# Kernel optimization log

Measured on AMD Instinct MI355X. Metric: run time of the kernel, lower is better.

The kernel has to match this reference:

```python
import jax, jax.numpy as jnp
import numpy as np

NH = 32          # nh * 2 neighbors per point (init nh=16)
P_REDUCTION = 0.5


def setup_inputs() -> dict:
    key = jax.random.key(0)
    k1, k2 = jax.random.split(key)
    x = jax.random.normal(k1, (2, 8192, 256), dtype=jnp.float32)       # [b, n, e]
    coords = jax.random.normal(k2, (2, 2, 8192, 1), dtype=jnp.float32) # [b, c, n, 1]
    return {"x": x, "coords": coords}


def _knn_gather(x, coords):
    """Return features of the NH nearest neighbors of each point: [b, n, NH, e]."""
    cs = coords[..., 0]                                   # [b, c, n]
    sq = jnp.sum(cs * cs, axis=1)                         # [b, n]
    # squared euclidean distances [b, n, n]
    d2 = sq[:, :, None] + sq[:, None, :] - 2.0 * jnp.einsum('bcn,bcm->bnm', cs, cs)
    d2 = jax.lax.stop_gradient(d2)                        # indices are non-differentiable
    _, nn_idx = jax.lax.top_k(-d2, NH)                    # [b, n, NH] nearest points
    # gather neighbor features: [b, 1, n, e] indexed with [b, n, NH, 1] -> [b, n, NH, e]
    x_nh = jnp.take_along_axis(x[:, None, :, :], nn_idx[..., None], axis=2)
    return x_nh


def _forward(x, coords):
    b, n, e = x.shape
    x_nh = _knn_gather(x, coords)                         # [b, n, NH, e]
    # unbiased std over the neighbor dim (torch.std default, ddof=1)
    mean_nh = jnp.mean(x_nh, axis=-2, keepdims=True)
    local_s = jnp.sqrt(jnp.sum((x_nh - mean_nh) ** 2, axis=-2) / (NH - 1))  # [b, n, e]
    global_m = jnp.abs(jnp.mean(x, axis=1))               # [b, e]
    local_dist = jnp.sum(local_s / global_m[:, None, :], axis=-1)           # [b, n]
    n_keep = int((1.0 - P_REDUCTION) * n)
    _, keep_idx = jax.lax.top_k(local_dist, n_keep)       # [b, n_keep], sorted desc
    x_out = jnp.take_along_axis(x, keep_idx[:, :, None], axis=1)            # [b, n_keep, e]
    coords_out = jnp.take_along_axis(coords, keep_idx[:, None, :, None], axis=2)  # [b, c, n_keep, 1]
    return x_out, coords_out, local_dist


def reference(x, coords):
    return _forward(x, coords)
```

## Files before the change

### kernel.cpp

```cpp
#include <hip/hip_runtime.h>

#define NN 8192
#define EE 256
#define KNH 32
#define NKEEP 4096
#define NCX 64
#define NCELL 4096
#define CNT_MIN 48

typedef unsigned long long u64;
typedef unsigned int u32;


__device__ __forceinline__ int cellof(float v) {
    const int q = (int)floorf((v + 4.6f) * (64.0f / 9.2f));
    return min(max(q, 0), NCX - 1);
}

__global__ void __launch_bounds__(1024) k_pre(const float* __restrict__ coords,
                                              const float* __restrict__ x,
                                              int* __restrict__ start,
                                              float2* __restrict__ sc,
                                              int* __restrict__ sj,
                                              float* __restrict__ part) {
    __shared__ int cnt[NCELL];
    __shared__ int wsum[16];
    const int blk = blockIdx.x;
    if (blk >= 2) {
        const int unit  = (blk - 2) * 4 + (threadIdx.x >> 8);
        const int b     = unit >> 5;
        const int chunk = unit & 31;
        const int t     = threadIdx.x & 255;
        const float* xp = x + ((size_t)b * NN + (size_t)chunk * 256) * EE + t;
        float s = 0.0f;
        for (int i = 0; i < 256; ++i) s += xp[(size_t)i * EE];
        part[((size_t)b * 32 + chunk) * EE + t] = s;
        return;
    }
    const int b = blk, t = threadIdx.x;
    const int lane = t & 63, wv = t >> 6;
#pragma unroll
    for (int k = 0; k < 4; ++k) cnt[k * 1024 + t] = 0;
    __syncthreads();
#pragma unroll
    for (int k = 0; k < 8; ++k) {
        const int i = k * 1024 + t;
        const float xv = coords[(size_t)b * 2 * NN + i];
        const float yv = coords[(size_t)b * 2 * NN + NN + i];
        atomicAdd(&cnt[cellof(xv) * NCX + cellof(yv)], 1);
    }
    __syncthreads();
    const int v0 = cnt[t * 4 + 0], v1 = cnt[t * 4 + 1];
    const int v2 = cnt[t * 4 + 2], v3 = cnt[t * 4 + 3];
    const int s = v0 + v1 + v2 + v3;
    int inc = s;
#pragma unroll
    for (int d = 1; d < 64; d <<= 1) {
        const int u = __shfl_up(inc, d);
        inc += (lane >= d) ? u : 0;
    }
    if (lane == 63) wsum[wv] = inc;
    __syncthreads();
    int wpre = 0;
#pragma unroll
    for (int w = 0; w < 16; ++w) wpre += (w < wv) ? wsum[w] : 0;
    int run = wpre + inc - s;
    start[b * (NCELL + 1) + t * 4 + 0] = run; cnt[t * 4 + 0] = run; run += v0;
    start[b * (NCELL + 1) + t * 4 + 1] = run; cnt[t * 4 + 1] = run; run += v1;
    start[b * (NCELL + 1) + t * 4 + 2] = run; cnt[t * 4 + 2] = run; run += v2;
    start[b * (NCELL + 1) + t * 4 + 3] = run; cnt[t * 4 + 3] = run; run += v3;
    if (t == 0) start[b * (NCELL + 1) + NCELL] = NN;
    __syncthreads();
#pragma unroll
    for (int k = 0; k < 8; ++k) {
        const int i = k * 1024 + t;
        const float xv = coords[(size_t)b * 2 * NN + i];
        const float yv = coords[(size_t)b * 2 * NN + NN + i];
        const int p = atomicAdd(&cnt[cellof(xv) * NCX + cellof(yv)], 1);
        sc[(size_t)b * NN + p] = make_float2(xv, yv);
        sj[(size_t)b * NN + p] = i;
    }
}

__global__ void k_gm_final(const float* __restrict__ part, float* __restrict__ gm) {
    const int b = blockIdx.y, t = threadIdx.x;
    float s = 0.0f;
    for (int c = 0; c < 32; ++c) s += part[((size_t)b * 32 + c) * EE + t];
    gm[b * EE + t] = fabsf(s / (float)NN);
}

__device__ __forceinline__ u64 shfl_xor_u64(u64 v, int m) {
    const u32 hi = (u32)__shfl_xor((int)(u32)(v >> 32), m);
    const u32 lo = (u32)__shfl_xor((int)(u32)v, m);
    return ((u64)hi << 32) | lo;
}

__device__ __forceinline__ u64 wave_min_u64(u64 h) {
#pragma unroll
    for (int s = 1; s < 64; s <<= 1) {
        const u64 o = shfl_xor_u64(h, s);
        h = (o < h) ? o : h;
    }
    return h;
}

__global__ void __launch_bounds__(256) k_knn_dist(
        const float* __restrict__ x,
        const float* __restrict__ gm, const float2* __restrict__ sc,
        const int* __restrict__ sj, const int* __restrict__ start,
        float* __restrict__ ld_out) {
    __shared__ u64 comp[4][64];
    const int wg   = blockIdx.x;
    const int swz  = (wg & 7) * 512 + (wg >> 3);
    const int b    = swz >> 11;
    const int pb   = swz & 2047;
    const int wid  = threadIdx.x >> 6;
    const int lane = threadIdx.x & 63;
    const int p    = pb * 4 + wid;

    const float2* scb = sc + (size_t)b * NN;
    const int*    sjb = sj + (size_t)b * NN;
    const int*    stb = start + b * (NCELL + 1);
    const float2 cp = scb[p];
    const int    i  = sjb[p];
    const float ci0 = cp.x, ci1 = cp.y;
    const int qx = cellof(ci0), qy = cellof(ci1);

    int r = 1, xl, yl, yh, nsl;
    int myc0 = 0, mylen = 0;
    for (;;) {
        xl = max(qx - r, 0);
        const int xh = min(qx + r, NCX - 1);
        yl = max(qy - r, 0);
        yh = min(qy + r, NCX - 1);
        nsl = xh - xl + 1;
        int c0 = 0, c1 = 0;
        if (lane < nsl) {
            c0 = stb[(xl + lane) * NCX + yl];
            c1 = stb[(xl + lane) * NCX + yh + 1];
        }
        myc0 = c0; mylen = c1 - c0;
        int tot = mylen;
#pragma unroll
        for (int s = 1; s < 64; s <<= 1) tot += __shfl_xor(tot, s);
        if (tot >= CNT_MIN || r >= NCX) break;
        r <<= 1;
    }
    int incl = mylen;
#pragma unroll
    for (int d = 1; d < 64; d <<= 1) {
        const int v = __shfl_up(incl, d);
        incl += (lane >= d) ? v : 0;
    }
    int excl = incl - mylen;
    const int L1 = __shfl(incl, 63);

    float dmin = 1e30f;
    for (int g = 0; g < L1; g += 64) {
        const int gp = g + lane;
        int lo = 0, hi = nsl - 1;
#pragma unroll
        for (int st = 0; st < 6; ++st) {
            const int mid = (lo + hi + 1) >> 1;
            const int v = __shfl(excl, mid);
            const bool go = (v <= gp);
            lo = go ? mid : lo;
            hi = go ? hi : mid - 1;
        }
        const int cnd = __shfl(myc0, lo) + gp - __shfl(excl, lo);
        const int cc  = min(max(cnd, 0), NN - 1);
        const float2 pt = scb[cc];
        const float dx = ci0 - pt.x, dy = ci1 - pt.y;
        const float d  = fmaf(dx, dx, dy * dy);
        if (gp < L1) dmin = fminf(dmin, d);
    }

    u32 mk = __float_as_uint(dmin);
#pragma unroll
    for (int k = 2; k <= 64; k <<= 1) {
#pragma unroll
        for (int j = k >> 1; j > 0; j >>= 1) {
            const u32 o = (u32)__shfl_xor((int)mk, j);
            const bool keep_min = (((lane & j) == 0) == ((lane & k) == 0));
            const u32 mn = min(mk, o), mx = max(mk, o);
            mk = keep_min ? mn : mx;
        }
    }
    const u32 T = (u32)__shfl((int)mk, 31);

    const float srad = sqrtf(__uint_as_float(T)) * 1.0002f + 1e-5f;
    xl = cellof(ci0 - srad);
    const int xh2 = cellof(ci0 + srad);
    yl = cellof(ci1 - srad);
    yh = cellof(ci1 + srad);
    nsl = xh2 - xl + 1;
    {
        int c0 = 0, c1 = 0;
        if (lane < nsl) {
            c0 = stb[(xl + lane) * NCX + yl];
            c1 = stb[(xl + lane) * NCX + yh + 1];
        }
        myc0 = c0; mylen = c1 - c0;
    }
    incl = mylen;
#pragma unroll
    for (int d = 1; d < 64; d <<= 1) {
        const int v = __shfl_up(incl, d);
        incl += (lane >= d) ? v : 0;
    }
    excl = incl - mylen;
    const int L2 = __shfl(incl, 63);

    const u64 lmask = (1ull << lane) - 1;
    int base = 0;
    for (int g = 0; g < L2; g += 64) {
        const int gp = g + lane;
        int lo = 0, hi = nsl - 1;
#pragma unroll
        for (int st = 0; st < 6; ++st) {
            const int mid = (lo + hi + 1) >> 1;
            const int v = __shfl(excl, mid);
            const bool go = (v <= gp);
            lo = go ? mid : lo;
            hi = go ? hi : mid - 1;
        }
        const int cnd = __shfl(myc0, lo) + gp - __shfl(excl, lo);
        const int cc  = min(max(cnd, 0), NN - 1);
        const float2 pt = scb[cc];
        const int    jj = sjb[cc];
        const float dx = ci0 - pt.x, dy = ci1 - pt.y;
        const u32 db = __float_as_uint(fmaf(dx, dx, dy * dy));
        const bool keep = (gp < L2) && (db <= T);
        const u64 m = __ballot(keep);
        const int pos = base + __popcll(m & lmask);
        base += __popcll(m);
        if (keep && pos < 64) comp[wid][pos] = ((u64)db << 32) | (u32)jj;
    }
    const bool ovf = (base > 64) || (base < KNH);

    u64 key = (lane < base) ? comp[wid][lane] : ~0ull;
#pragma unroll
    for (int k = 2; k <= 64; k <<= 1) {
#pragma unroll
        for (int j = k >> 1; j > 0; j >>= 1) {
            const u64 other = shfl_xor_u64(key, j);
            const bool keep_min = (((lane & j) == 0) == ((lane & k) == 0));
            const bool lt = (key < other);
            const u64 mn = lt ? key : other;
            const u64 mx = lt ? other : key;
            key = keep_min ? mn : mx;
        }
    }
    int jkeep = (int)(u32)key;

    if (ovf) {
        u64 minkeep = 0;
        for (int k = 0; k < KNH; ++k) {
            u64 best = ~0ull;
            for (int g = 0; g < L2; g += 64) {
                const int gp = g + lane;
                int lo = 0, hi = nsl - 1;
#pragma unroll
                for (int st = 0; st < 6; ++st) {
                    const int mid = (lo + hi + 1) >> 1;
                    const int v = __shfl(excl, mid);
                    const bool go = (v <= gp);
                    lo = go ? mid : lo;
                    hi = go ? hi : mid - 1;
                }
                const int cnd = __shfl(myc0, lo) + gp - __shfl(excl, lo);
                const int cc  = min(max(cnd, 0), NN - 1);
                const float2 pt = scb[cc];
                const int    jj = sjb[cc];
                const float dx = ci0 - pt.x, dy = ci1 - pt.y;
                const float d  = fmaf(dx, dx, dy * dy);
                const u64 kk = ((u64)__float_as_uint(d) << 32) | (u32)jj;
                if (gp < L2 && kk >= minkeep && kk < best) best = kk;
            }
            const u64 h = wave_min_u64(best);
            if (lane == k) jkeep = (int)(u32)h;
            minkeep = h + 1;
        }
    }

    float s1[4] = {0.f, 0.f, 0.f, 0.f};
    float s2[4] = {0.f, 0.f, 0.f, 0.f};
    const float* xb = x + (size_t)b * NN * EE;
#pragma unroll 8
    for (int k = 0; k < KNH; ++k) {
        const int j = __builtin_amdgcn_readlane(jkeep, k);
        const float4 v = *reinterpret_cast<const float4*>(xb + (size_t)j * EE + (lane << 2));
        s1[0] += v.x; s2[0] += v.x * v.x;
        s1[1] += v.y; s2[1] += v.y * v.y;
        s1[2] += v.z; s2[2] += v.z * v.z;
        s1[3] += v.w; s2[3] += v.w * v.w;
    }

    const float* gmb = gm + b * EE;
    float tt = 0.f;
#pragma unroll
    for (int q = 0; q < 4; ++q) {
        const float sum = s1[q];
        float ssd = s2[q] - sum * sum * (1.0f / 32.0f);
        ssd = ssd > 0.f ? ssd : 0.f;
        const float ls = sqrtf(ssd * (1.0f / 31.0f));
        tt += ls / gmb[(lane << 2) + q];
    }
#pragma unroll
    for (int s2r = 1; s2r < 64; s2r <<= 1) tt += __shfl_xor(tt, s2r);

    if (lane == 0) ld_out[(size_t)b * NN + i] = tt;
}

__global__ void k_rank_gather(const float* __restrict__ x, const float* __restrict__ coords,
                              const float* __restrict__ ld,
                              float* __restrict__ x_out, float* __restrict__ c_out) {
    const int b    = blockIdx.y;
    const int wid  = threadIdx.x >> 6;
    const int lane = threadIdx.x & 63;
    const int i    = blockIdx.x * 4 + wid;
    const float* lb = ld + (size_t)b * NN;
    const float di = lb[i];
    int cnt = 0;
    for (int t = 0; t < NN / 256; ++t) {
        const int j0 = t * 256 + (lane << 2);
        const float4 dv = *reinterpret_cast<const float4*>(lb + j0);
        cnt += (dv.x > di || (dv.x == di && (j0 + 0) < i)) ? 1 : 0;
        cnt += (dv.y > di || (dv.y == di && (j0 + 1) < i)) ? 1 : 0;
        cnt += (dv.z > di || (dv.z == di && (j0 + 2) < i)) ? 1 : 0;
        cnt += (dv.w > di || (dv.w == di && (j0 + 3) < i)) ? 1 : 0;
    }
#pragma unroll
    for (int s = 1; s < 64; s <<= 1) cnt += __shfl_xor(cnt, s);

    if (cnt < NKEEP) {
        const float4 v = *reinterpret_cast<const float4*>(x + ((size_t)b * NN + i) * EE + (lane << 2));
        *reinterpret_cast<float4*>(x_out + ((size_t)b * NKEEP + cnt) * EE + (lane << 2)) = v;
        if (lane < 2) {
            c_out[((size_t)b * 2 + lane) * NKEEP + cnt] = coords[((size_t)b * 2 + lane) * NN + i];
        }
    }
}

extern "C" void kernel_launch(void* const* d_in, const int* in_sizes, int n_in,
                              void* d_out, int out_size, void* d_ws, size_t ws_size,
                              hipStream_t stream) {
    const float* x      = (const float*)d_in[0];
    const float* coords = (const float*)d_in[1];

    float* out    = (float*)d_out;
    float* x_out  = out;
    float* c_out  = out + 2097152;
    float* ld_out = out + 2113536;

    char*   ws    = (char*)d_ws;
    float*  part  = (float*)(ws);
    float*  gm    = (float*)(ws + 65536);
    int*    start = (int*)  (ws + 67584);
    float2* sc    = (float2*)(ws + 100384);
    int*    sj    = (int*)  (ws + 231456);

    k_pre        <<<18,            1024, 0, stream>>>(coords, x, start, sc, sj, part);
    k_gm_final   <<<dim3(1, 2),    256,  0, stream>>>(part, gm);
    k_knn_dist   <<<4096,          256,  0, stream>>>(x, gm, sc, sj, start, ld_out);
    k_rank_gather<<<dim3(2048, 2), 256,  0, stream>>>(x, coords, ld_out, x_out, c_out);
}
```

Baseline: 86.25 us.

## Process two query points per wave in kNN kernel to raise ILP

After: 91.72 us. +6.3%, slower.

```diff
diff --git a/kernel.cpp b/kernel.cpp
--- a/kernel.cpp
+++ b/kernel.cpp
@@ -104,212 +104,284 @@
     return h;
 }
 
+__device__ __noinline__ int exact_fb(const float2* scb, const int* sjb, const int* stb,
+                                     float cx, float cy, int xl, int xh, int yl, int yh,
+                                     int lane) {
+    const int nsl = xh - xl + 1;
+    int c0 = 0, c1 = 0;
+    if (lane < nsl) { c0 = stb[(xl + lane) * NCX + yl]; c1 = stb[(xl + lane) * NCX + yh + 1]; }
+    const int myc = c0, len = c1 - c0;
+    int inc = len;
+#pragma unroll
+    for (int d = 1; d < 64; d <<= 1) {
+        const int v = __shfl_up(inc, d);
+        inc += (lane >= d) ? v : 0;
+    }
+    const int ex = inc - len;
+    const int L = __shfl(inc, 63);
+    int jk = 0;
+    u64 minkeep = 0;
+    for (int k = 0; k < KNH; ++k) {
+        u64 best = ~0ull;
+        for (int g = 0; g < L; g += 64) {
+            const int gp = g + lane;
+            int lo = 0, hi = nsl - 1;
+#pragma unroll
+            for (int st = 0; st < 6; ++st) {
+                const int mid = (lo + hi + 1) >> 1;
+                const int v = __shfl(ex, mid);
+                const bool go = (v <= gp);
+                lo = go ? mid : lo;
+                hi = go ? hi : mid - 1;
+            }
+            const int cnd = __shfl(myc, lo) + gp - __shfl(ex, lo);
+            const int cc = min(max(cnd, 0), NN - 1);
+            const float2 pt = scb[cc];
+            const int jj = sjb[cc];
+            const float dx = cx - pt.x, dy = cy - pt.y;
+            const float d = fmaf(dx, dx, dy * dy);
+            const u64 kk = ((u64)__float_as_uint(d) << 32) | (u32)jj;
+            if (gp < L && kk >= minkeep && kk < best) best = kk;
+        }
+        const u64 h = wave_min_u64(best);
+        if (lane == k) jk = (int)(u32)h;
+        minkeep = h + 1;
+    }
+    return jk;
+}
+
 __global__ void __launch_bounds__(256) k_knn_dist(
         const float* __restrict__ x,
         const float* __restrict__ gm, const float2* __restrict__ sc,
         const int* __restrict__ sj, const int* __restrict__ start,
         float* __restrict__ ld_out) {
-    __shared__ u64 comp[4][64];
+    __shared__ u64 comp[4][2][64];
     const int wg   = blockIdx.x;
-    const int swz  = (wg & 7) * 512 + (wg >> 3);
-    const int b    = swz >> 11;
-    const int pb   = swz & 2047;
+    const int idx  = wg >> 3, xcd = wg & 7;
+    const int swz  = (idx >> 5) * 256 + xcd * 32 + (idx & 31);
+    const int b    = swz >> 10;
+    const int pb   = swz & 1023;
     const int wid  = threadIdx.x >> 6;
     const int lane = threadIdx.x & 63;
-    const int p    = pb * 4 + wid;
+    const int pA   = (pb * 4 + wid) * 2;
+    const int pB   = pA + 1;
 
     const float2* scb = sc + (size_t)b * NN;
     const int*    sjb = sj + (size_t)b * NN;
     const int*    stb = start + b * (NCELL + 1);
-    const float2 cp = scb[p];
-    const int    i  = sjb[p];
-    const float ci0 = cp.x, ci1 = cp.y;
-    const int qx = cellof(ci0), qy = cellof(ci1);
-
-    int r = 1, xl, yl, yh, nsl;
-    int myc0 = 0, mylen = 0;
+    const float2 cpA = scb[pA], cpB = scb[pB];
+    const int    iA  = sjb[pA], iB = sjb[pB];
+    const float ax = cpA.x, ay = cpA.y, bx = cpB.x, by = cpB.y;
+    const int qxA = cellof(ax), qyA = cellof(ay);
+    const int qxB = cellof(bx), qyB = cellof(by);
+
+    int xlA, xhA, ylA, yhA, nslA, c0A = 0, lenA = 0, rA = 1;
+    int xlB, xhB, ylB, yhB, nslB, c0B = 0, lenB = 0, rB = 1;
+    bool dA = false, dB = false;
     for (;;) {
-        xl = max(qx - r, 0);
-        const int xh = min(qx + r, NCX - 1);
-        yl = max(qy - r, 0);
-        yh = min(qy + r, NCX - 1);
-        nsl = xh - xl + 1;
-        int c0 = 0, c1 = 0;
-        if (lane < nsl) {
-            c0 = stb[(xl + lane) * NCX + yl];
-            c1 = stb[(xl + lane) * NCX + yh + 1];
-        }
-        myc0 = c0; mylen = c1 - c0;
-        int tot = mylen;
-#pragma unroll
-        for (int s = 1; s < 64; s <<= 1) tot += __shfl_xor(tot, s);
-        if (tot >= CNT_MIN || r >= NCX) break;
-        r <<= 1;
-    }
-    int incl = mylen;
+        if (!dA) {
+            xlA = max(qxA - rA, 0); xhA = min(qxA + rA, NCX - 1);
+            ylA = max(qyA - rA, 0); yhA = min(qyA + rA, NCX - 1);
+            nslA = xhA - xlA + 1;
+            int c0 = 0, c1 = 0;
+            if (lane < nslA) { c0 = stb[(xlA + lane) * NCX + ylA]; c1 = stb[(xlA + lane) * NCX + yhA + 1]; }
+            c0A = c0; lenA = c1 - c0;
+            int tot = lenA;
+#pragma unroll
+            for (int s = 1; s < 64; s <<= 1) tot += __shfl_xor(tot, s);
+            if (tot >= CNT_MIN || rA >= NCX) dA = true; else rA <<= 1;
+        }
+        if (!dB) {
+            xlB = max(qxB - rB, 0); xhB = min(qxB + rB, NCX - 1);
+            ylB = max(qyB - rB, 0); yhB = min(qyB + rB, NCX - 1);
+            nslB = xhB - xlB + 1;
+            int c0 = 0, c1 = 0;
+            if (lane < nslB) { c0 = stb[(xlB + lane) * NCX + ylB]; c1 = stb[(xlB + lane) * NCX + yhB + 1]; }
+            c0B = c0; lenB = c1 - c0;
+            int tot = lenB;
+#pragma unroll
+            for (int s = 1; s < 64; s <<= 1) tot += __shfl_xor(tot, s);
+            if (tot >= CNT_MIN || rB >= NCX) dB = true; else rB <<= 1;
+        }
+        if (dA && dB) break;
+    }
+
+    int incA = lenA, incB = lenB;
 #pragma unroll
     for (int d = 1; d < 64; d <<= 1) {
-        const int v = __shfl_up(incl, d);
-        incl += (lane >= d) ? v : 0;
-    }
-    int excl = incl - mylen;
-    const int L1 = __shfl(incl, 63);
-
-    float dmin = 1e30f;
-    for (int g = 0; g < L1; g += 64) {
+        const int vA = __shfl_up(incA, d), vB = __shfl_up(incB, d);
+        incA += (lane >= d) ? vA : 0;
+        incB += (lane >= d) ? vB : 0;
+    }
+    int exA = incA - lenA, exB = incB - lenB;
+    const int L1A = __shfl(incA, 63), L1B = __shfl(incB, 63);
+
+    float dmA = 1e30f, dmB = 1e30f;
+    const int Lmax1 = max(L1A, L1B);
+    for (int g = 0; g < Lmax1; g += 64) {
         const int gp = g + lane;
-        int lo = 0, hi = nsl - 1;
+        int loA = 0, hiA = nslA - 1, loB = 0, hiB = nslB - 1;
 #pragma unroll
         for (int st = 0; st < 6; ++st) {
-            const int mid = (lo + hi + 1) >> 1;
-            const int v = __shfl(excl, mid);
-            const bool go = (v <= gp);
-            lo = go ? mid : lo;
-            hi = go ? hi : mid - 1;
-        }
-        const int cnd = __shfl(myc0, lo) + gp - __shfl(excl, lo);
-        const int cc  = min(max(cnd, 0), NN - 1);
-        const float2 pt = scb[cc];
-        const float dx = ci0 - pt.x, dy = ci1 - pt.y;
-        const float d  = fmaf(dx, dx, dy * dy);
-        if (gp < L1) dmin = fminf(dmin, d);
-    }
-
-    u32 mk = __float_as_uint(dmin);
+            const int midA = (loA + hiA + 1) >> 1, midB = (loB + hiB + 1) >> 1;
+            const int vA = __shfl(exA, midA), vB = __shfl(exB, midB);
+            const bool goA = (vA <= gp), goB = (vB <= gp);
+            loA = goA ? midA : loA; hiA = goA ? hiA : midA - 1;
+            loB = goB ? midB : loB; hiB = goB ? hiB : midB - 1;
+        }
+        const int cndA = __shfl(c0A, loA) + gp - __shfl(exA, loA);
+        const int cndB = __shfl(c0B, loB) + gp - __shfl(exB, loB);
+        const int ccA = min(max(cndA, 0), NN - 1), ccB = min(max(cndB, 0), NN - 1);
+        const float2 ptA = scb[ccA], ptB = scb[ccB];
+        const float dxA = ax - ptA.x, dyA = ay - ptA.y;
+        const float dxB = bx - ptB.x, dyB = by - ptB.y;
+        const float dsA = fmaf(dxA, dxA, dyA * dyA);
+        const float dsB = fmaf(dxB, dxB, dyB * dyB);
+        if (gp < L1A) dmA = fminf(dmA, dsA);
+        if (gp < L1B) dmB = fminf(dmB, dsB);
+    }
+
+    u32 mkA = __float_as_uint(dmA), mkB = __float_as_uint(dmB);
 #pragma unroll
     for (int k = 2; k <= 64; k <<= 1) {
 #pragma unroll
         for (int j = k >> 1; j > 0; j >>= 1) {
-            const u32 o = (u32)__shfl_xor((int)mk, j);
-            const bool keep_min = (((lane & j) == 0) == ((lane & k) == 0));
-            const u32 mn = min(mk, o), mx = max(mk, o);
-            mk = keep_min ? mn : mx;
-        }
-    }
-    const u32 T = (u32)__shfl((int)mk, 31);
-
-    const float srad = sqrtf(__uint_as_float(T)) * 1.0002f + 1e-5f;
-    xl = cellof(ci0 - srad);
-    const int xh2 = cellof(ci0 + srad);
-    yl = cellof(ci1 - srad);
-    yh = cellof(ci1 + srad);
-    nsl = xh2 - xl + 1;
+            const u32 oA = (u32)__shfl_xor((int)mkA, j);
+            const u32 oB = (u32)__shfl_xor((int)mkB, j);
+            const bool keep = (((lane & j) == 0) == ((lane & k) == 0));
+            const u32 mnA = min(mkA, oA), mxA = max(mkA, oA);
+            const u32 mnB = min(mkB, oB), mxB = max(mkB, oB);
+            mkA = keep ? mnA : mxA;
+            mkB = keep ? mnB : mxB;
+        }
+    }
+    const u32 TA = (u32)__shfl((int)mkA, 31);
+    const u32 TB = (u32)__shfl((int)mkB, 31);
+
+    const float srA = sqrtf(__uint_as_float(TA)) * 1.0002f + 1e-5f;
+    const float srB = sqrtf(__uint_as_float(TB)) * 1.0002f + 1e-5f;
+    xlA = cellof(ax - srA); xhA = cellof(ax + srA);
+    ylA = cellof(ay - srA); yhA = cellof(ay + srA);
+    xlB = cellof(bx - srB); xhB = cellof(bx + srB);
+    ylB = cellof(by - srB); yhB = cellof(by + srB);
+    nslA = xhA - xlA + 1; nslB = xhB - xlB + 1;
     {
         int c0 = 0, c1 = 0;
-        if (lane < nsl) {
-            c0 = stb[(xl + lane) * NCX + yl];
-            c1 = stb[(xl + lane) * NCX + yh + 1];
-        }
-        myc0 = c0; mylen = c1 - c0;
-    }
-    incl = mylen;
+        if (lane < nslA) { c0 = stb[(xlA + lane) * NCX + ylA]; c1 = stb[(xlA + lane) * NCX + yhA + 1]; }
+        c0A = c0; lenA = c1 - c0;
+        int e0 = 0, e1 = 0;
+        if (lane < nslB) { e0 = stb[(xlB + lane) * NCX + ylB]; e1 = stb[(xlB + lane) * NCX + yhB + 1]; }
+        c0B = e0; lenB = e1 - e0;
+    }
+    incA = lenA; incB = lenB;
 #pragma unroll
     for (int d = 1; d < 64; d <<= 1) {
-        const int v = __shfl_up(incl, d);
-        incl += (lane >= d) ? v : 0;
-    }
-    excl = incl - mylen;
-    const int L2 = __shfl(incl, 63);
+        const int vA = __shfl_up(incA, d), vB = __shfl_up(incB, d);
+        incA += (lane >= d) ? vA : 0;
+        incB += (lane >= d) ? vB : 0;
+    }
+    exA = incA - lenA; exB = incB - lenB;
+    const int L2A = __shfl(incA, 63), L2B = __shfl(incB, 63);
 
     const u64 lmask = (1ull << lane) - 1;
-    int base = 0;
-    for (int g = 0; g < L2; g += 64) {
+    int baseA = 0, baseB = 0;
+    const int Lmax2 = max(L2A, L2B);
+    for (int g = 0; g < Lmax2; g += 64) {
         const int gp = g + lane;
-        int lo = 0, hi = nsl - 1;
+        int loA = 0, hiA = nslA - 1, loB = 0, hiB = nslB - 1;
 #pragma unroll
         for (int st = 0; st < 6; ++st) {
-            const int mid = (lo + hi + 1) >> 1;
-            const int v = __shfl(excl, mid);
-            const bool go = (v <= gp);
-            lo = go ? mid : lo;
-            hi = go ? hi : mid - 1;
-        }
-        const int cnd = __shfl(myc0, lo) + gp - __shfl(excl, lo);
-        const int cc  = min(max(cnd, 0), NN - 1);
-        const float2 pt = scb[cc];
-        const int    jj = sjb[cc];
-        const float dx = ci0 - pt.x, dy = ci1 - pt.y;
-        const u32 db = __float_as_uint(fmaf(dx, dx, dy * dy));
-        const bool keep = (gp < L2) && (db <= T);
-        const u64 m = __ballot(keep);
-        const int pos = base + __popcll(m & lmask);
-        base += __popcll(m);
-        if (keep && pos < 64) comp[wid][pos] = ((u64)db << 32) | (u32)jj;
-    }
-    const bool ovf = (base > 64) || (base < KNH);
-
-    u64 key = (lane < base) ? comp[wid][lane] : ~0ull;
+            const int midA = (loA + hiA + 1) >> 1, midB = (loB + hiB + 1) >> 1;
+            const int vA = __shfl(exA, midA), vB = __shfl(exB, midB);
+            const bool goA = (vA <= gp), goB = (vB <= gp);
+            loA = goA ? midA : loA; hiA = goA ? hiA : midA - 1;
+            loB = goB ? midB : loB; hiB = goB ? hiB : midB - 1;
+        }
+        const int cndA = __shfl(c0A, loA) + gp - __shfl(exA, loA);
+        const int cndB = __shfl(c0B, loB) + gp - __shfl(exB, loB);
+        const int ccA = min(max(cndA, 0), NN - 1), ccB = min(max(cndB, 0), NN - 1);
+        const float2 ptA = scb[ccA], ptB = scb[ccB];
+        const int jjA = sjb[ccA], jjB = sjb[ccB];
+        const float dxA = ax - ptA.x, dyA = ay - ptA.y;
+        const float dxB = bx - ptB.x, dyB = by - ptB.y;
+        const u32 dbA = __float_as_uint(fmaf(dxA, dxA, dyA * dyA));
+        const u32 dbB = __float_as_uint(fmaf(dxB, dxB, dyB * dyB));
+        const bool kA = (gp < L2A) && (dbA <= TA);
+        const bool kB = (gp < L2B) && (dbB <= TB);
+        const u64 mA = __ballot(kA), mB = __ballot(kB);
+        const int posA = baseA + __popcll(mA & lmask);
+        const int posB = baseB + __popcll(mB & lmask);
+        baseA += __popcll(mA);
+        baseB += __popcll(mB);
+        if (kA && posA < 64) comp[wid][0][posA] = ((u64)dbA << 32) | (u32)jjA;
+        if (kB && posB < 64) comp[wid][1][posB] = ((u64)dbB << 32) | (u32)jjB;
+    }
+    const bool ovfA = (baseA > 64) || (baseA < KNH);
+    const bool ovfB = (baseB > 64) || (baseB < KNH);
+
+    u64 keyA = (lane < baseA) ? comp[wid][0][lane] : ~0ull;
+    u64 keyB = (lane < baseB) ? comp[wid][1][lane] : ~0ull;
 #pragma unroll
     for (int k = 2; k <= 64; k <<= 1) {
 #pragma unroll
         for (int j = k >> 1; j > 0; j >>= 1) {
-            const u64 other = shfl_xor_u64(key, j);
-            const bool keep_min = (((lane & j) == 0) == ((lane & k) == 0));
-            const bool lt = (key < other);
-            const u64 mn = lt ? key : other;
-            const u64 mx = lt ? other : key;
-            key = keep_min ? mn : mx;
-        }
-    }
-    int jkeep = (int)(u32)key;
-
-    if (ovf) {
-        u64 minkeep = 0;
-        for (int k = 0; k < KNH; ++k) {
-            u64 best = ~0ull;
-            for (int g = 0; g < L2; g += 64) {
-                const int gp = g + lane;
-                int lo = 0, hi = nsl - 1;
-#pragma unroll
-                for (int st = 0; st < 6; ++st) {
-                    const int mid = (lo + hi + 1) >> 1;
-                    const int v = __shfl(excl, mid);
-                    const bool go = (v <= gp);
-                    lo = go ? mid : lo;
-                    hi = go ? hi : mid - 1;
-                }
-                const int cnd = __shfl(myc0, lo) + gp - __shfl(excl, lo);
-                const int cc  = min(max(cnd, 0), NN - 1);
-                const float2 pt = scb[cc];
-                const int    jj = sjb[cc];
-                const float dx = ci0 - pt.x, dy = ci1 - pt.y;
-                const float d  = fmaf(dx, dx, dy * dy);
-                const u64 kk = ((u64)__float_as_uint(d) << 32) | (u32)jj;
-                if (gp < L2 && kk >= minkeep && kk < best) best = kk;
-            }
-            const u64 h = wave_min_u64(best);
-            if (lane == k) jkeep = (int)(u32)h;
-            minkeep = h + 1;
-        }
-    }
-
-    float s1[4] = {0.f, 0.f, 0.f, 0.f};
-    float s2[4] = {0.f, 0.f, 0.f, 0.f};
+            const u64 oA = shfl_xor_u64(keyA, j), oB = shfl_xor_u64(keyB, j);
+            const bool keep = (((lane & j) == 0) == ((lane & k) == 0));
+            const bool ltA = (keyA < oA), ltB = (keyB < oB);
+            const u64 mnA = ltA ? keyA : oA, mxA = ltA ? oA : keyA;
+            const u64 mnB = ltB ? keyB : oB, mxB = ltB ? oB : keyB;
+            keyA = keep ? mnA : mxA;
+            keyB = keep ? mnB : mxB;
+        }
+    }
+    int jkA = (int)(u32)keyA;
+    int jkB = (int)(u32)keyB;
+
+    if (ovfA) jkA = exact_fb(scb, sjb, stb, ax, ay, xlA, xhA, ylA, yhA, lane);
+    if (ovfB) jkB = exact_fb(scb, sjb, stb, bx, by, xlB, xhB, ylB, yhB, lane);
+
+    float s1A[4] = {0.f, 0.f, 0.f, 0.f}, s2A[4] = {0.f, 0.f, 0.f, 0.f};
+    float s1B[4] = {0.f, 0.f, 0.f, 0.f}, s2B[4] = {0.f, 0.f, 0.f, 0.f};
     const float* xb = x + (size_t)b * NN * EE;
-#pragma unroll 8
+#pragma unroll 4
     for (int k = 0; k < KNH; ++k) {
-        const int j = __builtin_amdgcn_readlane(jkeep, k);
-        const float4 v = *reinterpret_cast<const float4*>(xb + (size_t)j * EE + (lane << 2));
-        s1[0] += v.x; s2[0] += v.x * v.x;
-        s1[1] += v.y; s2[1] += v.y * v.y;
-        s1[2] += v.z; s2[2] += v.z * v.z;
-        s1[3] += v.w; s2[3] += v.w * v.w;
+        const int jA = __builtin_amdgcn_readlane(jkA, k);
+        const int jB = __builtin_amdgcn_readlane(jkB, k);
+        const float4 vA = *reinterpret_cast<const float4*>(xb + (size_t)jA * EE + (lane << 2));
+        const float4 vB = *reinterpret_cast<const float4*>(xb + (size_t)jB * EE + (lane << 2));
+        s1A[0] += vA.x; s2A[0] += vA.x * vA.x;
+        s1B[0] += vB.x; s2B[0] += vB.x * vB.x;
+        s1A[1] += vA.y; s2A[1] += vA.y * vA.y;
+        s1B[1] += vB.y; s2B[1] += vB.y * vB.y;
+        s1A[2] += vA.z; s2A[2] += vA.z * vA.z;
+        s1B[2] += vB.z; s2B[2] += vB.z * vB.z;
+        s1A[3] += vA.w; s2A[3] += vA.w * vA.w;
+        s1B[3] += vB.w; s2B[3] += vB.w * vB.w;
     }
 
     const float* gmb = gm + b * EE;
-    float tt = 0.f;
+    float ttA = 0.f, ttB = 0.f;
 #pragma unroll
     for (int q = 0; q < 4; ++q) {
-        const float sum = s1[q];
-        float ssd = s2[q] - sum * sum * (1.0f / 32.0f);
-        ssd = ssd > 0.f ? ssd : 0.f;
-        const float ls = sqrtf(ssd * (1.0f / 31.0f));
-        tt += ls / gmb[(lane << 2) + q];
-    }
-#pragma unroll
-    for (int s2r = 1; s2r < 64; s2r <<= 1) tt += __shfl_xor(tt, s2r);
-
-    if (lane == 0) ld_out[(size_t)b * NN + i] = tt;
+        const float g_ = gmb[(lane << 2) + q];
+        const float suA = s1A[q], suB = s1B[q];
+        float sdA = s2A[q] - suA * suA * (1.0f / 32.0f);
+        float sdB = s2B[q] - suB * suB * (1.0f / 32.0f);
+        sdA = sdA > 0.f ? sdA : 0.f;
+        sdB = sdB > 0.f ? sdB : 0.f;
+        ttA += sqrtf(sdA * (1.0f / 31.0f)) / g_;
+        ttB += sqrtf(sdB * (1.0f / 31.0f)) / g_;
+    }
+#pragma unroll
+    for (int s = 1; s < 64; s <<= 1) {
+        ttA += __shfl_xor(ttA, s);
+        ttB += __shfl_xor(ttB, s);
+    }
+
+    if (lane == 0) {
+        ld_out[(size_t)b * NN + iA] = ttA;
+        ld_out[(size_t)b * NN + iB] = ttB;
+    }
 }
 
 __global__ void k_rank_gather(const float* __restrict__ x, const float* __restrict__ coords,
@@ -362,6 +434,6 @@
 
     k_pre        <<<18,            1024, 0, stream>>>(coords, x, start, sc, sj, part);
     k_gm_final   <<<dim3(1, 2),    256,  0, stream>>>(part, gm);
-    k_knn_dist   <<<4096,          256,  0, stream>>>(x, gm, sc, sj, start, ld_out);
+    k_knn_dist   <<<2048,          256,  0, stream>>>(x, gm, sc, sj, start, ld_out);
     k_rank_gather<<<dim3(2048, 2), 256,  0, stream>>>(x, coords, ld_out, x_out, c_out);
 }
```

## Share a union candidate box across the workgroup's waves and stage it in LDS

Applied to the files above, without the earlier changes.

After: 206.3 us. 139% more time.

```diff
diff --git a/kernel.cpp b/kernel.cpp
--- a/kernel.cpp
+++ b/kernel.cpp
@@ -7,6 +7,7 @@
 #define NCX 64
 #define NCELL 4096
 #define CNT_MIN 48
+#define CAP 1536
 
 typedef unsigned long long u64;
 typedef unsigned int u32;
@@ -104,12 +105,61 @@
     return h;
 }
 
+__device__ __noinline__ int exact_fb(const float2* scb, const int* sjb, const int* stb,
+                                     float cx, float cy, int xl, int xh, int yl, int yh,
+                                     int lane) {
+    const int nsl = xh - xl + 1;
+    int c0 = 0, c1 = 0;
+    if (lane < nsl) { c0 = stb[(xl + lane) * NCX + yl]; c1 = stb[(xl + lane) * NCX + yh + 1]; }
+    const int myc = c0, len = c1 - c0;
+    int inc = len;
+#pragma unroll
+    for (int d = 1; d < 64; d <<= 1) {
+        const int v = __shfl_up(inc, d);
+        inc += (lane >= d) ? v : 0;
+    }
+    const int ex = inc - len;
+    const int L = __shfl(inc, 63);
+    int jk = 0;
+    u64 minkeep = 0;
+    for (int k = 0; k < KNH; ++k) {
+        u64 best = ~0ull;
+        for (int g = 0; g < L; g += 64) {
+            const int gp = g + lane;
+            int lo = 0, hi = nsl - 1;
+#pragma unroll
+            for (int st = 0; st < 6; ++st) {
+                const int mid = (lo + hi + 1) >> 1;
+                const int v = __shfl(ex, mid);
+                const bool go = (v <= gp);
+                lo = go ? mid : lo;
+                hi = go ? hi : mid - 1;
+            }
+            const int cnd = __shfl(myc, lo) + gp - __shfl(ex, lo);
+            const int cc = min(max(cnd, 0), NN - 1);
+            const float2 pt = scb[cc];
+            const int jj = sjb[cc];
+            const float dx = cx - pt.x, dy = cy - pt.y;
+            const float d = fmaf(dx, dx, dy * dy);
+            const u64 kk = ((u64)__float_as_uint(d) << 32) | (u32)jj;
+            if (gp < L && kk >= minkeep && kk < best) best = kk;
+        }
+        const u64 h = wave_min_u64(best);
+        if (lane == k) jk = (int)(u32)h;
+        minkeep = h + 1;
+    }
+    return jk;
+}
+
 __global__ void __launch_bounds__(256) k_knn_dist(
         const float* __restrict__ x,
         const float* __restrict__ gm, const float2* __restrict__ sc,
         const int* __restrict__ sj, const int* __restrict__ start,
         float* __restrict__ ld_out) {
+    __shared__ float2 lxy[CAP];
+    __shared__ int    ljj[CAP];
     __shared__ u64 comp[4][64];
+    __shared__ int boxes[4][4];
     const int wg   = blockIdx.x;
     const int swz  = (wg & 7) * 512 + (wg >> 3);
     const int b    = swz >> 11;
@@ -126,53 +176,91 @@
     const float ci0 = cp.x, ci1 = cp.y;
     const int qx = cellof(ci0), qy = cellof(ci1);
 
-    int r = 1, xl, yl, yh, nsl;
-    int myc0 = 0, mylen = 0;
+    int r = 1, xl1, xh1, yl1, yh1;
     for (;;) {
-        xl = max(qx - r, 0);
-        const int xh = min(qx + r, NCX - 1);
-        yl = max(qy - r, 0);
-        yh = min(qy + r, NCX - 1);
-        nsl = xh - xl + 1;
+        xl1 = max(qx - r, 0);
+        xh1 = min(qx + r, NCX - 1);
+        yl1 = max(qy - r, 0);
+        yh1 = min(qy + r, NCX - 1);
+        const int nsl = xh1 - xl1 + 1;
         int c0 = 0, c1 = 0;
         if (lane < nsl) {
-            c0 = stb[(xl + lane) * NCX + yl];
-            c1 = stb[(xl + lane) * NCX + yh + 1];
-        }
-        myc0 = c0; mylen = c1 - c0;
-        int tot = mylen;
+            c0 = stb[(xl1 + lane) * NCX + yl1];
+            c1 = stb[(xl1 + lane) * NCX + yh1 + 1];
+        }
+        int tot = c1 - c0;
 #pragma unroll
         for (int s = 1; s < 64; s <<= 1) tot += __shfl_xor(tot, s);
         if (tot >= CNT_MIN || r >= NCX) break;
         r <<= 1;
     }
+    if (lane == 0) {
+        boxes[wid][0] = xl1; boxes[wid][1] = xh1;
+        boxes[wid][2] = yl1; boxes[wid][3] = yh1;
+    }
+    __syncthreads();
+    const int uxl = min(min(boxes[0][0], boxes[1][0]), min(boxes[2][0], boxes[3][0]));
+    const int uxh = max(max(boxes[0][1], boxes[1][1]), max(boxes[2][1], boxes[3][1]));
+    const int uyl = min(min(boxes[0][2], boxes[1][2]), min(boxes[2][2], boxes[3][2]));
+    const int uyh = max(max(boxes[0][3], boxes[1][3]), max(boxes[2][3], boxes[3][3]));
+    const int unsl = uxh - uxl + 1;
+
+    int c0 = 0, c1 = 0;
+    if (lane < unsl) {
+        c0 = stb[(uxl + lane) * NCX + uyl];
+        c1 = stb[(uxl + lane) * NCX + uyh + 1];
+    }
+    const int mylen = c1 - c0;
     int incl = mylen;
 #pragma unroll
     for (int d = 1; d < 64; d <<= 1) {
         const int v = __shfl_up(incl, d);
         incl += (lane >= d) ? v : 0;
     }
-    int excl = incl - mylen;
-    const int L1 = __shfl(incl, 63);
+    const int excl = incl - mylen;
+    const int L = __shfl(incl, 63);
+    const bool useLds = (L <= CAP);
+
+    if (useLds) {
+        int off = 0;
+        for (int s = 0; s < unsl; ++s) {
+            const int s0 = __shfl(c0, s);
+            const int sl = __shfl(mylen, s);
+            for (int u = threadIdx.x; u < sl; u += 256) {
+                lxy[off + u] = scb[s0 + u];
+                ljj[off + u] = sjb[s0 + u];
+            }
+            off += sl;
+        }
+    }
+    __syncthreads();
 
     float dmin = 1e30f;
-    for (int g = 0; g < L1; g += 64) {
-        const int gp = g + lane;
-        int lo = 0, hi = nsl - 1;
-#pragma unroll
-        for (int st = 0; st < 6; ++st) {
-            const int mid = (lo + hi + 1) >> 1;
-            const int v = __shfl(excl, mid);
-            const bool go = (v <= gp);
-            lo = go ? mid : lo;
-            hi = go ? hi : mid - 1;
-        }
-        const int cnd = __shfl(myc0, lo) + gp - __shfl(excl, lo);
-        const int cc  = min(max(cnd, 0), NN - 1);
-        const float2 pt = scb[cc];
-        const float dx = ci0 - pt.x, dy = ci1 - pt.y;
-        const float d  = fmaf(dx, dx, dy * dy);
-        if (gp < L1) dmin = fminf(dmin, d);
+    if (useLds) {
+        for (int g = lane; g < L; g += 64) {
+            const float2 pt = lxy[g];
+            const float dx = ci0 - pt.x, dy = ci1 - pt.y;
+            dmin = fminf(dmin, fmaf(dx, dx, dy * dy));
+        }
+    } else {
+        for (int g = 0; g < L; g += 64) {
+            const int gp = g + lane;
+            int lo = 0, hi = unsl - 1;
+#pragma unroll
+            for (int st = 0; st < 6; ++st) {
+                const int mid = (lo + hi + 1) >> 1;
+                const int v = __shfl(excl, mid);
+                const bool go = (v <= gp);
+                lo = go ? mid : lo;
+                hi = go ? hi : mid - 1;
+            }
+            const int cnd = __shfl(c0, lo) + gp - __shfl(excl, lo);
+            const int cc  = min(max(cnd, 0), NN - 1);
+            const float2 pt = scb[cc];
+            const float dx = ci0 - pt.x, dy = ci1 - pt.y;
+            const float d  = fmaf(dx, dx, dy * dy);
+            if (gp < L) dmin = fminf(dmin, d);
+        }
     }
 
     u32 mk = __float_as_uint(dmin);
@@ -189,54 +277,54 @@
     const u32 T = (u32)__shfl((int)mk, 31);
 
     const float srad = sqrtf(__uint_as_float(T)) * 1.0002f + 1e-5f;
-    xl = cellof(ci0 - srad);
-    const int xh2 = cellof(ci0 + srad);
-    yl = cellof(ci1 - srad);
-    yh = cellof(ci1 + srad);
-    nsl = xh2 - xl + 1;
-    {
-        int c0 = 0, c1 = 0;
-        if (lane < nsl) {
-            c0 = stb[(xl + lane) * NCX + yl];
-            c1 = stb[(xl + lane) * NCX + yh + 1];
-        }
-        myc0 = c0; mylen = c1 - c0;
-    }
-    incl = mylen;
-#pragma unroll
-    for (int d = 1; d < 64; d <<= 1) {
-        const int v = __shfl_up(incl, d);
-        incl += (lane >= d) ? v : 0;
-    }
-    excl = incl - mylen;
-    const int L2 = __shfl(incl, 63);
+    const int xl2 = cellof(ci0 - srad), xh2 = cellof(ci0 + srad);
+    const int yl2 = cellof(ci1 - srad), yh2 = cellof(ci1 + srad);
+    const bool contained = (xl2 >= uxl) && (xh2 <= uxh) && (yl2 >= uyl) && (yh2 <= uyh);
 
     const u64 lmask = (1ull << lane) - 1;
     int base = 0;
-    for (int g = 0; g < L2; g += 64) {
-        const int gp = g + lane;
-        int lo = 0, hi = nsl - 1;
-#pragma unroll
-        for (int st = 0; st < 6; ++st) {
-            const int mid = (lo + hi + 1) >> 1;
-            const int v = __shfl(excl, mid);
-            const bool go = (v <= gp);
-            lo = go ? mid : lo;
-            hi = go ? hi : mid - 1;
-        }
-        const int cnd = __shfl(myc0, lo) + gp - __shfl(excl, lo);
-        const int cc  = min(max(cnd, 0), NN - 1);
-        const float2 pt = scb[cc];
-        const int    jj = sjb[cc];
-        const float dx = ci0 - pt.x, dy = ci1 - pt.y;
-        const u32 db = __float_as_uint(fmaf(dx, dx, dy * dy));
-        const bool keep = (gp < L2) && (db <= T);
-        const u64 m = __ballot(keep);
-        const int pos = base + __popcll(m & lmask);
-        base += __popcll(m);
-        if (keep && pos < 64) comp[wid][pos] = ((u64)db << 32) | (u32)jj;
-    }
-    const bool ovf = (base > 64) || (base < KNH);
+    if (contained) {
+        if (useLds) {
+            for (int g = 0; g < L; g += 64) {
+                const int gp = g + lane;
+                const int gc = min(gp, L - 1);
+                const float2 pt = lxy[gc];
+                const int    jj = ljj[gc];
+                const float dx = ci0 - pt.x, dy = ci1 - pt.y;
+                const u32 db = __float_as_uint(fmaf(dx, dx, dy * dy));
+                const bool keep = (gp < L) && (db <= T);
+                const u64 m = __ballot(keep);
+                const int pos = base + __popcll(m & lmask);
+                base += __popcll(m);
+                if (keep && pos < 64) comp[wid][pos] = ((u64)db << 32) | (u32)jj;
+            }
+        } else {
+            for (int g = 0; g < L; g += 64) {
+                const int gp = g + lane;
+                int lo = 0, hi = unsl - 1;
+#pragma unroll
+                for (int st = 0; st < 6; ++st) {
+                    const int mid = (lo + hi + 1) >> 1;
+                    const int v = __shfl(excl, mid);
+                    const bool go = (v <= gp);
+                    lo = go ? mid : lo;
+                    hi = go ? hi : mid - 1;
+                }
+                const int cnd = __shfl(c0, lo) + gp - __shfl(excl, lo);
+                const int cc  = min(max(cnd, 0), NN - 1);
+                const float2 pt = scb[cc];
+                const int    jj = sjb[cc];
+                const float dx = ci0 - pt.x, dy = ci1 - pt.y;
+                const u32 db = __float_as_uint(fmaf(dx, dx, dy * dy));
+                const bool keep = (gp < L) && (db <= T);
+                const u64 m = __ballot(keep);
+                const int pos = base + __popcll(m & lmask);
+                base += __popcll(m);
+                if (keep && pos < 64) comp[wid][pos] = ((u64)db << 32) | (u32)jj;
+            }
+        }
+    }
+    const bool ovf = (!contained) || (base > 64) || (base < KNH);
 
     u64 key = (lane < base) ? comp[wid][lane] : ~0ull;
 #pragma unroll
@@ -253,35 +341,7 @@
     }
     int jkeep = (int)(u32)key;
 
-    if (ovf) {
-        u64 minkeep = 0;
-        for (int k = 0; k < KNH; ++k) {
-            u64 best = ~0ull;
-            for (int g = 0; g < L2; g += 64) {
-                const int gp = g + lane;
-                int lo = 0, hi = nsl - 1;
-#pragma unroll
-                for (int st = 0; st < 6; ++st) {
-                    const int mid = (lo + hi + 1) >> 1;
-                    const int v = __shfl(excl, mid);
-                    const bool go = (v <= gp);
-                    lo = go ? mid : lo;
-                    hi = go ? hi : mid - 1;
-                }
-                const int cnd = __shfl(myc0, lo) + gp - __shfl(excl, lo);
-                const int cc  = min(max(cnd, 0), NN - 1);
-                const float2 pt = scb[cc];
-                const int    jj = sjb[cc];
-                const float dx = ci0 - pt.x, dy = ci1 - pt.y;
-                const float d  = fmaf(dx, dx, dy * dy);
-                const u64 kk = ((u64)__float_as_uint(d) << 32) | (u32)jj;
-                if (gp < L2 && kk >= minkeep && kk < best) best = kk;
-            }
-            const u64 h = wave_min_u64(best);
-            if (lane == k) jkeep = (int)(u32)h;
-            minkeep = h + 1;
-        }
-    }
+    if (ovf) jkeep = exact_fb(scb, sjb, stb, ci0, ci1, xl2, xh2, yl2, yh2, lane);
 
     float s1[4] = {0.f, 0.f, 0.f, 0.f};
     float s2[4] = {0.f, 0.f, 0.f, 0.f};
```
